# Kernel optimization log

Hardware: AMD Instinct MI355X
Metric: run time of the kernel (lower is better)

## Reference

```python
import jax, jax.numpy as jnp
import numpy as np

EMBED_DIM = 1024
HEAD_DIM = 128


def setup_inputs() -> dict:
    key = jax.random.key(0)
    k_x, k_qkv, k_out, k_b = jax.random.split(key, 4)
    x = jax.random.normal(k_x, (4, 4096, EMBED_DIM), dtype=jnp.float32)
    # torch Linear weights, stored as [in, out] so y = x @ W
    w_qkv = jax.random.normal(k_qkv, (EMBED_DIM, 3 * HEAD_DIM), dtype=jnp.float32) * (EMBED_DIM ** -0.5)
    w_out = jax.random.normal(k_out, (HEAD_DIM, EMBED_DIM), dtype=jnp.float32) * (HEAD_DIM ** -0.5)
    b_out = jax.random.normal(k_b, (EMBED_DIM,), dtype=jnp.float32) * 0.01
    return {"x": x, "w_qkv": w_qkv, "w_out": w_out, "b_out": b_out}


def reference(x, w_qkv, w_out, b_out):
    b, t, c = x.shape
    qkv = x @ w_qkv                                  # [b, t, 3*head_dim]
    q, k, v = jnp.split(qkv, 3, axis=-1)             # each [b, t, head_dim]
    # NOTE: original scales by embed_dim**-0.5 (c), not head_dim**-0.5
    wei = jnp.einsum('bqd,bkd->bqk', q, k) * (c ** -0.5)  # [b, t, t]
    causal = jnp.tril(jnp.ones((t, t), dtype=bool))
    wei = jnp.where(causal, wei, -jnp.inf)
    wei = jax.nn.softmax(wei, axis=-1)
    out = jnp.einsum('bqk,bkd->bqd', wei, v)         # [b, t, head_dim]
    return out @ w_out + b_out                       # [b, t, embed_dim]
```

## Files before the change

### kernel.cpp

```cpp
#include <hip/hip_runtime.h>
#include <hip/hip_bf16.h>

typedef __attribute__((ext_vector_type(8))) short short8;
typedef __attribute__((ext_vector_type(4))) float float4v;
typedef __attribute__((ext_vector_type(16))) float f32x16;
typedef __attribute__((ext_vector_type(4))) unsigned uint4v;

#define AS1(p) ((const __attribute__((address_space(1))) void*)(p))
#define AS3(p) ((__attribute__((address_space(3))) void*)(p))

#define NSPLIT 8

__device__ __forceinline__ ushort f2bf(float f) {
    union { float f; unsigned u; } v; v.f = f;
    unsigned u = v.u;
    unsigned r = (u + 0x7fffu + ((u >> 16) & 1u)) >> 16;
    return (ushort)r;
}
__device__ __forceinline__ float bf2f(ushort u) {
    union { unsigned u; float f; } v; v.u = ((unsigned)u) << 16;
    return v.f;
}

__global__ void transpose_cast(const float* __restrict__ in, ushort* __restrict__ out, int R, int C) {
    int idx = blockIdx.x * blockDim.x + threadIdx.x;
    if (idx >= R * C) return;
    int r = idx / C, c = idx - r * C;
    out[(size_t)c * R + r] = f2bf(in[idx]);
}

__device__ __forceinline__ void stage128x64(const ushort* gbase, int ld, ushort* lds, int tid) {
    const int wavebase = tid & 192;
#pragma unroll
    for (int j = 0; j < 4; ++j) {
        int idx = j * 256 + tid;
        int row = idx >> 3;
        int slot = idx & 7;
        int s = slot ^ (row & 7);
        const ushort* g = gbase + (size_t)row * ld + s * 8;
        int ldsoff = (j * 256 + wavebase) * 16;
        __builtin_amdgcn_global_load_lds(AS1(g), AS3((char*)lds + ldsoff), 16, 0, 0);
    }
}

__device__ __forceinline__ void compute64(const ushort* As, const ushort* Bs,
                                          int wr, int wc, int row16, int grp,
                                          float4v acc[4][4]) {
    const char* Ab = (const char*)As;
    const char* Bb = (const char*)Bs;
#pragma unroll
    for (int kk = 0; kk < 2; ++kk) {
        short8 a[4], b[4];
        const int sw = row16 & 7;
#pragma unroll
        for (int m = 0; m < 4; ++m)
            a[m] = *(const short8*)(Ab + (wr * 64 + m * 16 + row16) * 128 + (((kk * 4 + grp) ^ sw) << 4));
#pragma unroll
        for (int n = 0; n < 4; ++n)
            b[n] = *(const short8*)(Bb + (wc * 64 + n * 16 + row16) * 128 + (((kk * 4 + grp) ^ sw) << 4));
#pragma unroll
        for (int m = 0; m < 4; ++m)
#pragma unroll
            for (int n = 0; n < 4; ++n)
                acc[m][n] = __builtin_amdgcn_mfma_f32_16x16x32_bf16(a[m], b[n], acc[m][n], 0, 0, 0);
    }
}

__device__ __forceinline__ void compute64x128(const ushort* As, const ushort* Bs,
                                              int wr, int wc, int row16, int grp,
                                              float4v acc[2][4]) {
    const char* Ab = (const char*)As;
    const char* Bb = (const char*)Bs;
#pragma unroll
    for (int kk = 0; kk < 2; ++kk) {
        short8 a[2], b[4];
        const int sw = row16 & 7;
#pragma unroll
        for (int m = 0; m < 2; ++m)
            a[m] = *(const short8*)(Ab + (wr * 32 + m * 16 + row16) * 128 + (((kk * 4 + grp) ^ sw) << 4));
#pragma unroll
        for (int n = 0; n < 4; ++n)
            b[n] = *(const short8*)(Bb + (wc * 64 + n * 16 + row16) * 128 + (((kk * 4 + grp) ^ sw) << 4));
#pragma unroll
        for (int m = 0; m < 2; ++m)
#pragma unroll
            for (int n = 0; n < 4; ++n)
                acc[m][n] = __builtin_amdgcn_mfma_f32_16x16x32_bf16(a[m], b[n], acc[m][n], 0, 0, 0);
    }
}

__global__ __launch_bounds__(256) void gemm_qkv(const float* __restrict__ x,
                                                const ushort* __restrict__ wT,
                                                ushort* __restrict__ Qm,
                                                ushort* __restrict__ Km,
                                                ushort* __restrict__ Vt) {
    __shared__ ushort S[12288];
    ushort* As = S;
    ushort* Bs = S + 4096;
    const int tid = threadIdx.x;
    const int lane = tid & 63, w = tid >> 6;
    const int row16 = lane & 15, grp = lane >> 4;
    const int wr = w >> 1, wc = w & 1;
    const int mt = blockIdx.x * 64;
    const int by = blockIdx.y;
    const int n0 = by * 128;

    float4v acc[2][4];
#pragma unroll
    for (int m = 0; m < 2; ++m)
#pragma unroll
        for (int n = 0; n < 4; ++n) acc[m][n] = (float4v){0.f, 0.f, 0.f, 0.f};

#define LOAD_A(KT)                                                         \
    _Pragma("unroll") for (int j = 0; j < 2; ++j) {                        \
        int idx = j * 256 + tid;                                           \
        int row = idx >> 3, slot = idx & 7;                                \
        const float* src = x + (size_t)(mt + row) * 1024 + (KT) + slot * 8;\
        va[j][0] = *(const float4*)(src);                                  \
        va[j][1] = *(const float4*)(src + 4);                              \
    }

    float4 va[2][2];
    LOAD_A(0);

    for (int kt = 0; kt < 1024; kt += 64) {
        stage128x64(wT + (size_t)n0 * 1024 + kt, 1024, Bs, tid);
#pragma unroll
        for (int j = 0; j < 2; ++j) {
            int idx = j * 256 + tid;
            int row = idx >> 3, slot = idx & 7;
            short8 h;
            h[0] = f2bf(va[j][0].x); h[1] = f2bf(va[j][0].y);
            h[2] = f2bf(va[j][0].z); h[3] = f2bf(va[j][0].w);
            h[4] = f2bf(va[j][1].x); h[5] = f2bf(va[j][1].y);
            h[6] = f2bf(va[j][1].z); h[7] = f2bf(va[j][1].w);
            *(short8*)((char*)As + row * 128 + ((slot ^ (row & 7)) << 4)) = h;
        }
        __syncthreads();
        if (kt + 64 < 1024) LOAD_A(kt + 64);
        compute64x128(As, Bs, wr, wc, row16, grp, acc);
        __syncthreads();
    }
#undef LOAD_A

    if (by == 2) {
#pragma unroll
        for (int m = 0; m < 2; ++m)
#pragma unroll
            for (int i = 0; i < 4; ++i) {
                int trow = wr * 32 + m * 16 + grp * 4 + i;
#pragma unroll
                for (int n = 0; n < 4; ++n) {
                    int d = wc * 64 + n * 16 + row16;
                    S[d * 72 + trow] = f2bf(acc[m][n][i]);
                }
            }
        __syncthreads();
        const int b = mt >> 12, tloc = mt & 4095;
#pragma unroll
        for (int j = 0; j < 4; ++j) {
            int chunk = j * 256 + tid;
            int d = chunk >> 3, tc = chunk & 7;
            *(short8*)(Vt + ((size_t)(b * 128 + d)) * 4096 + tloc + tc * 8) =
                *(const short8*)(S + d * 72 + tc * 8);
        }
        return;
    }

    const float oscale = (by == 0) ? (0.03125f * 1.44269504f) : 1.0f;
    ushort* dst = (by == 0) ? Qm : Km;
#pragma unroll
    for (int m = 0; m < 2; ++m)
#pragma unroll
        for (int i = 0; i < 4; ++i) {
            int row = mt + wr * 32 + m * 16 + grp * 4 + i;
#pragma unroll
            for (int n = 0; n < 4; ++n) {
                int coll = wc * 64 + n * 16 + row16;
                dst[(size_t)row * 128 + coll] = f2bf(acc[m][n][i] * oscale);
            }
        }
}

__global__ __launch_bounds__(256, 3) void attn_split(const ushort* __restrict__ Qm,
                                                     const ushort* __restrict__ Km,
                                                     const ushort* __restrict__ Vt,
                                                     ushort* __restrict__ Opart,
                                                     float* __restrict__ Lpart) {
    __shared__ ushort Ks[2][32 * 128];
    __shared__ ushort Vs[2][128 * 32];

    const int tid = threadIdx.x;
    const int lane = tid & 63, w = tid >> 6;
    const int key31 = lane & 31;
    const int g = lane >> 5;

    const int bx = blockIdx.x;
    const int xcd = bx & 7;
    const int b = xcd >> 1;
    const int combo = ((bx >> 3) << 1) | (xcd & 1);
    const int qb = 31 - (combo >> 3);
    const int s = combo & 7;

    const int ext = 4 * qb + 4;
    const int t0 = (s * ext) >> 3;
    const int t1 = ((s + 1) * ext) >> 3;

    const int qtile32 = qb * 4 + w;
    const int qt0 = qtile32 * 32;
    const int qmax = qt0 + 31;
    const size_t pbase = ((size_t)b * 128 + qtile32) * NSPLIT + s;
    float* mlL = Lpart + pbase * 32;

    if (t0 >= t1) {
        if (lane < 32) mlL[lane] = 0.f;
        return;
    }

    const int qrow = qt0 + key31;
    const ushort* qbp = Qm + ((size_t)(b * 4096 + qrow)) * 128 + g * 8;
    short8 qf[8];
#pragma unroll
    for (int sl = 0; sl < 8; ++sl)
        qf[sl] = *reinterpret_cast<const short8*>(qbp + sl * 16);

    f32x16 o[4];
#pragma unroll
    for (int d4 = 0; d4 < 4; ++d4)
#pragma unroll
        for (int r = 0; r < 16; ++r) o[d4][r] = 0.f;
    float lrun = 0.f;

    const ushort* kbase = Km + (size_t)b * 4096 * 128;
    const ushort* vbase = Vt + (size_t)b * 128 * 4096;

#define STAGE_KV(KVT, BUF)                                                                     \
    {                                                                                          \
        const ushort* kb_ = kbase + (size_t)(KVT) * 128;                                       \
        _Pragma("unroll") for (int j = 0; j < 2; ++j) {                                        \
            int idx = j * 256 + tid;                                                           \
            int row = idx >> 4, c = idx & 15;                                                  \
            int sc_ = (c & 8) | ((c & 7) ^ (row & 7));                                         \
            __builtin_amdgcn_global_load_lds(AS1(kb_ + (size_t)row * 128 + sc_ * 8),           \
                AS3((char*)&Ks[BUF][0] + (j * 256 + (tid & 192)) * 16), 16, 0, 0);             \
        }                                                                                      \
        const ushort* vb_ = vbase + (KVT);                                                     \
        _Pragma("unroll") for (int j = 0; j < 2; ++j) {                                        \
            int idx = j * 256 + tid;                                                           \
            int row = idx >> 2, c = idx & 3;                                                   \
            int sc_ = c ^ ((row >> 1) & 3);                                                    \
            __builtin_amdgcn_global_load_lds(AS1(vb_ + (size_t)row * 4096 + sc_ * 8),          \
                AS3((char*)&Vs[BUF][0] + (j * 256 + (tid & 192)) * 16), 16, 0, 0);             \
        }                                                                                      \
    }

    STAGE_KV(t0 * 32, 0);

    int cur = 0;
    for (int t = t0; t < t1; ++t) {
        const int kvt = t * 32;
        __builtin_amdgcn_s_barrier();
        if (t + 1 < t1) {
            STAGE_KV((t + 1) * 32, cur ^ 1);
            asm volatile("s_waitcnt vmcnt(4)" ::: "memory");
        } else {
            asm volatile("s_waitcnt vmcnt(0)" ::: "memory");
        }
        __builtin_amdgcn_s_barrier();
        __builtin_amdgcn_sched_barrier(0);

        if (kvt <= qmax) {
            const char* Kb = (const char*)&Ks[cur][0];
            f32x16 st;
#pragma unroll
            for (int r = 0; r < 16; ++r) st[r] = 0.f;
            __builtin_amdgcn_s_setprio(1);
#pragma unroll
            for (int sl = 0; sl < 8; ++sl) {
                int c = sl * 2 + g;
                int sc_ = (c & 8) | ((c & 7) ^ (key31 & 7));
                short8 kfr = *(const short8*)(Kb + key31 * 256 + sc_ * 16);
                st = __builtin_amdgcn_mfma_f32_32x32x16_bf16(kfr, qf[sl], st, 0, 0, 0);
            }
            __builtin_amdgcn_s_setprio(0);
            if (kvt + 31 > qt0) {
#pragma unroll
                for (int r = 0; r < 16; ++r) {
                    int key = kvt + (r & 3) + 8 * (r >> 2) + 4 * g;
                    if (key > qrow) st[r] = -3e38f;
                }
            }
#pragma unroll
            for (int r = 0; r < 16; ++r) {
                float p = exp2f(st[r]);
                st[r] = p;
                lrun += p;
            }
            unsigned pk0, pk1, pk2, pk3, pk4, pk5, pk6, pk7;
            asm("v_cvt_pk_bf16_f32 %0, %1, %2" : "=v"(pk0) : "v"(st[0]),  "v"(st[1]));
            asm("v_cvt_pk_bf16_f32 %0, %1, %2" : "=v"(pk1) : "v"(st[2]),  "v"(st[3]));
            asm("v_cvt_pk_bf16_f32 %0, %1, %2" : "=v"(pk2) : "v"(st[4]),  "v"(st[5]));
            asm("v_cvt_pk_bf16_f32 %0, %1, %2" : "=v"(pk3) : "v"(st[6]),  "v"(st[7]));
            asm("v_cvt_pk_bf16_f32 %0, %1, %2" : "=v"(pk4) : "v"(st[8]),  "v"(st[9]));
            asm("v_cvt_pk_bf16_f32 %0, %1, %2" : "=v"(pk5) : "v"(st[10]), "v"(st[11]));
            asm("v_cvt_pk_bf16_f32 %0, %1, %2" : "=v"(pk6) : "v"(st[12]), "v"(st[13]));
            asm("v_cvt_pk_bf16_f32 %0, %1, %2" : "=v"(pk7) : "v"(st[14]), "v"(st[15]));
            asm volatile("v_permlane32_swap_b32 %0, %1" : "+v"(pk0), "+v"(pk2));
            asm volatile("v_permlane32_swap_b32 %0, %1" : "+v"(pk1), "+v"(pk3));
            asm volatile("v_permlane32_swap_b32 %0, %1" : "+v"(pk4), "+v"(pk6));
            asm volatile("v_permlane32_swap_b32 %0, %1" : "+v"(pk5), "+v"(pk7));
            union FW { uint4v u; short8 s; };
            FW f0; f0.u = (uint4v){pk0, pk1, pk2, pk3};
            FW f1; f1.u = (uint4v){pk4, pk5, pk6, pk7};
            short8 fa0 = f0.s;
            short8 fa1 = f1.s;
            const char* Vb = (const char*)&Vs[cur][0];
            __builtin_amdgcn_s_setprio(1);
#pragma unroll
            for (int d4 = 0; d4 < 4; ++d4) {
                int d = d4 * 32 + key31;
                int sw = (d >> 1) & 3;
                short8 v0 = *(const short8*)(Vb + d * 64 + ((0 * 2 + g) ^ sw) * 16);
                o[d4] = __builtin_amdgcn_mfma_f32_32x32x16_bf16(fa0, v0, o[d4], 0, 0, 0);
                short8 v1 = *(const short8*)(Vb + d * 64 + ((1 * 2 + g) ^ sw) * 16);
                o[d4] = __builtin_amdgcn_mfma_f32_32x32x16_bf16(fa1, v1, o[d4], 0, 0, 0);
            }
            __builtin_amdgcn_s_setprio(0);
        }
        cur ^= 1;
    }
#undef STAGE_KV

    lrun += __shfl_xor(lrun, 32);
    ushort* ob = Opart + pbase * 32 * 128;
#pragma unroll
    for (int d4 = 0; d4 < 4; ++d4)
#pragma unroll
        for (int r = 0; r < 16; ++r) {
            int qr = (r & 3) + 8 * (r >> 2) + 4 * g;
            ob[(size_t)qr * 128 + d4 * 32 + key31] = f2bf(o[d4][r]);
        }
    if (lane < 32) mlL[lane] = lrun;
}

__global__ __launch_bounds__(128) void attn_combine(const ushort* __restrict__ Opart,
                                                    const float* __restrict__ Lpart,
                                                    ushort* __restrict__ AO) {
    const int row = blockIdx.x;
    const int b = row >> 12, t = row & 4095;
    const int qtile = t >> 5, r = t & 31;
    const size_t sb = (((size_t)b * 128 + qtile) * NSPLIT);
    const int col = threadIdx.x;
    float acc = 0.f, denom = 0.f;
#pragma unroll
    for (int s = 0; s < NSPLIT; ++s) {
        float l = Lpart[(sb + s) * 32 + r];
        if (l > 0.f) {
            denom += l;
            acc += bf2f(Opart[((sb + s) * 32 + r) * 128 + col]);
        }
    }
    AO[(size_t)row * 128 + col] = f2bf(acc / denom);
}

__global__ __launch_bounds__(256) void gemm_out(const ushort* __restrict__ AO,
                                                const ushort* __restrict__ wT,
                                                const float* __restrict__ bias,
                                                float* __restrict__ out) {
    __shared__ ushort As[128 * 64];
    __shared__ ushort Bs[128 * 64];
    const int tid = threadIdx.x;
    const int lane = tid & 63, w = tid >> 6;
    const int row16 = lane & 15, grp = lane >> 4;
    const int wr = w >> 1, wc = w & 1;
    const int mt = blockIdx.x * 128;
    const int n0 = blockIdx.y * 128;

    float4v acc[4][4];
#pragma unroll
    for (int m = 0; m < 4; ++m)
#pragma unroll
        for (int n = 0; n < 4; ++n) acc[m][n] = (float4v){0.f, 0.f, 0.f, 0.f};

#pragma unroll
    for (int kt = 0; kt < 128; kt += 64) {
        stage128x64(AO + (size_t)mt * 128 + kt, 128, As, tid);
        stage128x64(wT + (size_t)n0 * 128 + kt, 128, Bs, tid);
        __syncthreads();
        compute64(As, Bs, wr, wc, row16, grp, acc);
        __syncthreads();
    }

#pragma unroll
    for (int n = 0; n < 4; ++n) {
        int col = n0 + wc * 64 + n * 16 + row16;
        float bv = bias[col];
#pragma unroll
        for (int m = 0; m < 4; ++m)
#pragma unroll
            for (int i = 0; i < 4; ++i) {
                int row = mt + wr * 64 + m * 16 + grp * 4 + i;
                out[(size_t)row * 1024 + col] = acc[m][n][i] + bv;
            }
    }
}

extern "C" void kernel_launch(void* const* d_in, const int* in_sizes, int n_in,
                              void* d_out, int out_size, void* d_ws, size_t ws_size,
                              hipStream_t stream) {
    const float* x     = (const float*)d_in[0];
    const float* w_qkv = (const float*)d_in[1];
    const float* w_out = (const float*)d_in[2];
    const float* b_out = (const float*)d_in[3];
    float* out = (float*)d_out;

    char* ws = (char*)d_ws;
    ushort* wqkvT = (ushort*)(ws + 33554432);
    ushort* woutT = (ushort*)(ws + 34340864);
    ushort* Qm    = (ushort*)(ws + 34603008);
    ushort* Km    = (ushort*)(ws + 38797312);
    ushort* Vt    = (ushort*)(ws + 42991616);
    ushort* AO    = (ushort*)(ws + 47185920);
    ushort* Opart = (ushort*)(ws);
    float* Lpart  = (float*)(ws + 51380224);

    transpose_cast<<<dim3((1024 * 384 + 255) / 256), dim3(256), 0, stream>>>(w_qkv, wqkvT, 1024, 384);
    transpose_cast<<<dim3((128 * 1024 + 255) / 256), dim3(256), 0, stream>>>(w_out, woutT, 128, 1024);

    gemm_qkv<<<dim3(256, 3), dim3(256), 0, stream>>>(x, wqkvT, Qm, Km, Vt);

    attn_split<<<dim3(1024), dim3(256), 0, stream>>>(Qm, Km, Vt, Opart, Lpart);
    attn_combine<<<dim3(16384), dim3(128), 0, stream>>>(Opart, Lpart, AO);

    gemm_out<<<dim3(128, 8), dim3(256), 0, stream>>>(AO, woutT, b_out, out);
}
```

Before: 105.3 us.

## Halve attention split count, merge weight transposes, use packed bf16 convert

Reduces the flash-decoding style key split from 8 to 4, so attention runs 512 blocks, each doing twice the keys, and there are fewer partial results to combine. Merges the two weight transpose-cast launches into one kernel to save a launch. Replaces scalar bf16 rounding in the QKV GEMM A-tile staging with packed v_cvt_pk_bf16_f32 inline asm. Fewer splits lower combine traffic and per-block overhead, but reduce parallelism and worsen load balance across CUs. The combine kernel is not visibly updated, so it is unclear whether it still assumes 8 partials.

After: 111.7 us. +6.2%, slower.

```diff
diff --git a/kernel.cpp b/kernel.cpp
--- a/kernel.cpp
+++ b/kernel.cpp
@@ -9,7 +9,7 @@
 #define AS1(p) ((const __attribute__((address_space(1))) void*)(p))
 #define AS3(p) ((__attribute__((address_space(3))) void*)(p))
 
-#define NSPLIT 8
+#define NSPLIT 4
 
 __device__ __forceinline__ ushort f2bf(float f) {
     union { float f; unsigned u; } v; v.f = f;
@@ -22,11 +22,19 @@
     return v.f;
 }
 
-__global__ void transpose_cast(const float* __restrict__ in, ushort* __restrict__ out, int R, int C) {
+__global__ void transpose_cast2(const float* __restrict__ wqkv, ushort* __restrict__ wqkvT,
+                                const float* __restrict__ wout, ushort* __restrict__ woutT) {
     int idx = blockIdx.x * blockDim.x + threadIdx.x;
-    if (idx >= R * C) return;
-    int r = idx / C, c = idx - r * C;
-    out[(size_t)c * R + r] = f2bf(in[idx]);
+    if (idx < 1024 * 384) {
+        int r = idx / 384, c = idx - r * 384;
+        wqkvT[(size_t)c * 1024 + r] = f2bf(wqkv[idx]);
+    } else {
+        int i2 = idx - 1024 * 384;
+        if (i2 < 128 * 1024) {
+            int r = i2 >> 10, c = i2 & 1023;
+            woutT[(size_t)c * 128 + r] = f2bf(wout[i2]);
+        }
+    }
 }
 
 __device__ __forceinline__ void stage128x64(const ushort* gbase, int ld, ushort* lds, int tid) {
@@ -129,12 +137,14 @@
         for (int j = 0; j < 2; ++j) {
             int idx = j * 256 + tid;
             int row = idx >> 3, slot = idx & 7;
-            short8 h;
-            h[0] = f2bf(va[j][0].x); h[1] = f2bf(va[j][0].y);
-            h[2] = f2bf(va[j][0].z); h[3] = f2bf(va[j][0].w);
-            h[4] = f2bf(va[j][1].x); h[5] = f2bf(va[j][1].y);
-            h[6] = f2bf(va[j][1].z); h[7] = f2bf(va[j][1].w);
-            *(short8*)((char*)As + row * 128 + ((slot ^ (row & 7)) << 4)) = h;
+            unsigned h0, h1, h2, h3;
+            asm("v_cvt_pk_bf16_f32 %0, %1, %2" : "=v"(h0) : "v"(va[j][0].x), "v"(va[j][0].y));
+            asm("v_cvt_pk_bf16_f32 %0, %1, %2" : "=v"(h1) : "v"(va[j][0].z), "v"(va[j][0].w));
+            asm("v_cvt_pk_bf16_f32 %0, %1, %2" : "=v"(h2) : "v"(va[j][1].x), "v"(va[j][1].y));
+            asm("v_cvt_pk_bf16_f32 %0, %1, %2" : "=v"(h3) : "v"(va[j][1].z), "v"(va[j][1].w));
+            union { uint4v u; short8 s; } hh;
+            hh.u = (uint4v){h0, h1, h2, h3};
+            *(short8*)((char*)As + row * 128 + ((slot ^ (row & 7)) << 4)) = hh.s;
         }
         __syncthreads();
         if (kt + 64 < 1024) LOAD_A(kt + 64);
@@ -199,12 +209,12 @@
     const int xcd = bx & 7;
     const int b = xcd >> 1;
     const int combo = ((bx >> 3) << 1) | (xcd & 1);
-    const int qb = 31 - (combo >> 3);
-    const int s = combo & 7;
+    const int qb = 31 - (combo >> 2);
+    const int s = combo & 3;
 
     const int ext = 4 * qb + 4;
-    const int t0 = (s * ext) >> 3;
-    const int t1 = ((s + 1) * ext) >> 3;
+    const int t0 = (s * ext) >> 2;
+    const int t1 = ((s + 1) * ext) >> 2;
 
     const int qtile32 = qb * 4 + w;
     const int qt0 = qtile32 * 32;
@@ -424,12 +434,11 @@
     ushort* Opart = (ushort*)(ws);
     float* Lpart  = (float*)(ws + 51380224);
 
-    transpose_cast<<<dim3((1024 * 384 + 255) / 256), dim3(256), 0, stream>>>(w_qkv, wqkvT, 1024, 384);
-    transpose_cast<<<dim3((128 * 1024 + 255) / 256), dim3(256), 0, stream>>>(w_out, woutT, 128, 1024);
+    transpose_cast2<<<dim3(2048), dim3(256), 0, stream>>>(w_qkv, wqkvT, w_out, woutT);
 
     gemm_qkv<<<dim3(256, 3), dim3(256), 0, stream>>>(x, wqkvT, Qm, Km, Vt);
 
-    attn_split<<<dim3(1024), dim3(256), 0, stream>>>(Qm, Km, Vt, Opart, Lpart);
+    attn_split<<<dim3(512), dim3(256), 0, stream>>>(Qm, Km, Vt, Opart, Lpart);
     attn_combine<<<dim3(16384), dim3(128), 0, stream>>>(Opart, Lpart, AO);
 
     gemm_out<<<dim3(128, 8), dim3(256), 0, stream>>>(AO, woutT, b_out, out);
```
